# Performance work log

Measured on AMD Instinct MI355X. Metric: run time of the kernel, lower is better.

The kernel has to match this reference:

```python
import jax, jax.numpy as jnp
import numpy as np

B, S, D, H = 4, 1024, 1024, 16
HD = D // H  # 64, even for RoPE


def _rope_tables(seq_len, head_dim):
    inv_freq = 1.0 / (10000.0 ** (jnp.arange(0, head_dim, 2, dtype=jnp.float32) / head_dim))
    pos = jnp.arange(seq_len, dtype=jnp.float32)
    ang = pos[:, None] * inv_freq[None, :]           # [S, HD/2]
    return jnp.cos(ang), jnp.sin(ang)


def _apply_rope(x, cos, sin):
    # x: [B, S, H, HD]; cos/sin: [S, HD/2] broadcast to [1, S, 1, HD/2]
    c = cos[None, :, None, :]
    s = sin[None, :, None, :]
    x1 = x[..., 0::2]
    x2 = x[..., 1::2]
    return jnp.concatenate([x1 * c - x2 * s, x1 * s + x2 * c], axis=-1)


def setup_inputs() -> dict:
    key = jax.random.key(0)
    ks = jax.random.split(key, 11)
    sc = 1.0 / np.sqrt(D)
    inp = {
        "query": jax.random.normal(ks[0], (B, S, D), jnp.float32),
        "key": jax.random.normal(ks[1], (B, S, D), jnp.float32),
        "value": jax.random.normal(ks[2], (B, S, D), jnp.float32),
        "mask": jnp.tril(jnp.ones((S, S), jnp.int32))[None, None],  # causal [1,1,S,S]
        "Wq": jax.random.normal(ks[3], (D, D), jnp.float32) * sc,
        "bq": jnp.zeros((D,), jnp.float32),
        "Wk": jax.random.normal(ks[4], (D, D), jnp.float32) * sc,
        "bk": jnp.zeros((D,), jnp.float32),
        "Wv": jax.random.normal(ks[5], (D, D), jnp.float32) * sc,
        "bv": jnp.zeros((D,), jnp.float32),
        "Wo": jax.random.normal(ks[6], (D, D), jnp.float32) * sc,
        "bo": jnp.zeros((D,), jnp.float32),
    }
    return inp


def reference(query, key, value, mask, Wq, bq, Wk, bk, Wv, bv, Wo, bo):
    Bq, Sq, _ = query.shape
    Sk = key.shape[1]
    q = (query @ Wq + bq).reshape(Bq, Sq, H, HD)
    k = (key @ Wk + bk).reshape(Bq, Sk, H, HD)
    v = (value @ Wv + bv).reshape(Bq, Sk, H, HD)
    cos, sin = _rope_tables(max(Sq, Sk), HD)
    q = _apply_rope(q, cos[:Sq], sin[:Sq])
    k = _apply_rope(k, cos[:Sk], sin[:Sk])
    scores = jnp.einsum("bqhd,bkhd->bhqk", q, k) / jnp.sqrt(jnp.float32(HD))
    scores = jnp.where(mask == 0, jnp.float32(-jnp.inf), scores)
    attn = jax.nn.softmax(scores, axis=-1)  # dropout p=0 (inference)
    ctx = jnp.einsum("bhqk,bkhd->bqhd", attn, v).reshape(Bq, Sq, D)
    return ctx @ Wo + bo
```

## Files before the change

### kernel.cpp

```cpp
#include <hip/hip_runtime.h>
#include <hip/hip_bf16.h>
#include <math.h>

#define B_DIM 4
#define S_DIM 1024
#define D_DIM 1024
#define H_DIM 16
#define HD_DIM 64
#define M_TOT 4096

typedef short short8 __attribute__((ext_vector_type(8)));
typedef float f32x4 __attribute__((ext_vector_type(4)));

__device__ inline float bf2f(short u)
{
    return __uint_as_float(((unsigned)(unsigned short)u) << 16);
}

__device__ inline void gload_lds16(const void* gsrc, void* lds)
{
    __builtin_amdgcn_global_load_lds(
        (const __attribute__((address_space(1))) unsigned int*)gsrc,
        (__attribute__((address_space(3))) unsigned int*)lds, 16, 0, 0);
}

__global__ __launch_bounds__(256) void rope_table_kernel(float* __restrict__ tab)
{
    const int t = blockIdx.x * 256 + threadIdx.x;
    const int pos = t >> 5, i = t & 31;
    float inv = powf(10000.0f, -(float)(2 * i) / 64.0f);
    float ang = (float)pos * inv;
    float s, c;
    sincosf(ang, &s, &c);
    tab[t] = c;
    tab[32768 + t] = s;
}

__global__ __launch_bounds__(256) void transpose4_to_bf16_kernel(
    const float* __restrict__ W0, const float* __restrict__ W1,
    const float* __restrict__ W2, const float* __restrict__ W3,
    __hip_bfloat16* __restrict__ T0, __hip_bfloat16* __restrict__ T1,
    __hip_bfloat16* __restrict__ T2, __hip_bfloat16* __restrict__ T3)
{
    const float* W = (blockIdx.z == 0) ? W0 : (blockIdx.z == 1) ? W1
                    : (blockIdx.z == 2) ? W2 : W3;
    __hip_bfloat16* T = (blockIdx.z == 0) ? T0 : (blockIdx.z == 1) ? T1
                       : (blockIdx.z == 2) ? T2 : T3;

    __shared__ float tile[32][33];
    const int tid = threadIdx.x;
    const int r = tid >> 3;
    const int c4 = (tid & 7) * 4;

    float4 v = *(const float4*)&W[(long)(blockIdx.y * 32 + r) * D_DIM + blockIdx.x * 32 + c4];
    tile[r][c4 + 0] = v.x;
    tile[r][c4 + 1] = v.y;
    tile[r][c4 + 2] = v.z;
    tile[r][c4 + 3] = v.w;
    __syncthreads();

    __hip_bfloat16 o[4];
    o[0] = __float2bfloat16(tile[c4 + 0][r]);
    o[1] = __float2bfloat16(tile[c4 + 1][r]);
    o[2] = __float2bfloat16(tile[c4 + 2][r]);
    o[3] = __float2bfloat16(tile[c4 + 3][r]);
    *(uint2*)&T[(long)(blockIdx.x * 32 + r) * D_DIM + blockIdx.y * 32 + c4] = *(uint2*)o;
}

__global__ __launch_bounds__(256, 3) void gemm_qkv_kernel(
    const float* __restrict__ Xq, const float* __restrict__ Xk,
    const float* __restrict__ Xv,
    const __hip_bfloat16* __restrict__ WtQ, const __hip_bfloat16* __restrict__ WtK,
    const __hip_bfloat16* __restrict__ WtV,
    const float* __restrict__ bq, const float* __restrict__ bk,
    const float* __restrict__ bv,
    __hip_bfloat16* __restrict__ Qo, __hip_bfloat16* __restrict__ Ko,
    __hip_bfloat16* __restrict__ Vto,
    const float* __restrict__ tab)
{
    __shared__ __align__(16) __hip_bfloat16 Al[2][128][40];
    __shared__ __align__(16) __hip_bfloat16 Bl[2][128][32];

    const int F = blockIdx.x + 8 * blockIdx.y + 256 * blockIdx.z;
    const int xcd = F & 7;
    const int sb = F >> 3;
    const int z = sb >> 5;
    const int n0 = (sb & 7) * 128;
    const int m0 = ((xcd << 2) | ((sb >> 3) & 3)) * 128;

    const float* X = (z == 0) ? Xq : (z == 1) ? Xk : Xv;
    const __hip_bfloat16* Wt = (z == 0) ? WtQ : (z == 1) ? WtK : WtV;
    const float* bias = (z == 0) ? bq : (z == 1) ? bk : bv;

    const int tid = threadIdx.x;
    const int l = tid & 63;
    const int w = tid >> 6;

    const int srow = w * 16 + (l >> 2);
    const int sk = ((l & 3) ^ ((l >> 2) & 3)) * 8;
    const __hip_bfloat16* Bbase = Wt + (long)(n0 + srow) * D_DIM + sk;

    const int arow = tid >> 1;
    const int ak = (tid & 1) * 16;
    const float* Af = X + (long)(m0 + arow) * D_DIM + ak;

    const int lrow = l & 15;
    const int kg = l >> 4;
    const int ksw = (kg ^ (lrow & 3)) * 8;
    const int wr = (w >> 1) * 64;
    const int wc = (w & 1) * 64;

    f32x4 acc[4][4];
#pragma unroll
    for (int i = 0; i < 4; ++i)
#pragma unroll
        for (int j = 0; j < 4; ++j) acc[i][j] = (f32x4){0.f, 0.f, 0.f, 0.f};

    {
        char* ldsB = (char*)&Bl[0][0][0] + w * 1024;
        gload_lds16(Bbase, ldsB);
        gload_lds16(Bbase + 64 * D_DIM, ldsB + 4096);
        float4 f0 = *(const float4*)(Af);
        float4 f1 = *(const float4*)(Af + 4);
        float4 f2 = *(const float4*)(Af + 8);
        float4 f3 = *(const float4*)(Af + 12);
        float fa[16] = {f0.x, f0.y, f0.z, f0.w, f1.x, f1.y, f1.z, f1.w,
                        f2.x, f2.y, f2.z, f2.w, f3.x, f3.y, f3.z, f3.w};
        __attribute__((aligned(16))) __hip_bfloat16 ab[16];
#pragma unroll
        for (int i = 0; i < 16; ++i) ab[i] = __float2bfloat16(fa[i]);
        *(short8*)&Al[0][arow][ak]     = ((const short8*)ab)[0];
        *(short8*)&Al[0][arow][ak + 8] = ((const short8*)ab)[1];
    }
    __syncthreads();

#pragma unroll 2
    for (int t = 0; t < 32; ++t) {
        const int cur = t & 1;
        const int nxt = cur ^ 1;
        const bool more = (t < 31);

        float4 f0, f1, f2, f3;
        if (more) {
            const int k0n = (t + 1) * 32;
            char* ldsB = (char*)&Bl[nxt][0][0] + w * 1024;
            gload_lds16(Bbase + k0n, ldsB);
            gload_lds16(Bbase + 64 * D_DIM + k0n, ldsB + 4096);
            f0 = *(const float4*)(Af + k0n);
            f1 = *(const float4*)(Af + k0n + 4);
            f2 = *(const float4*)(Af + k0n + 8);
            f3 = *(const float4*)(Af + k0n + 12);
        }

        short8 af[4], bf[4];
#pragma unroll
        for (int i = 0; i < 4; ++i)
            af[i] = *(const short8*)&Al[cur][wr + i * 16 + lrow][kg * 8];
#pragma unroll
        for (int j = 0; j < 4; ++j)
            bf[j] = *(const short8*)&Bl[cur][wc + j * 16 + lrow][ksw];
#pragma unroll
        for (int i = 0; i < 4; ++i)
#pragma unroll
            for (int j = 0; j < 4; ++j)
                acc[i][j] = __builtin_amdgcn_mfma_f32_16x16x32_bf16(
                    af[i], bf[j], acc[i][j], 0, 0, 0);

        if (more) {
            float fa[16] = {f0.x, f0.y, f0.z, f0.w, f1.x, f1.y, f1.z, f1.w,
                            f2.x, f2.y, f2.z, f2.w, f3.x, f3.y, f3.z, f3.w};
            __attribute__((aligned(16))) __hip_bfloat16 ab[16];
#pragma unroll
            for (int i = 0; i < 16; ++i) ab[i] = __float2bfloat16(fa[i]);
            *(short8*)&Al[nxt][arow][ak]     = ((const short8*)ab)[0];
            *(short8*)&Al[nxt][arow][ak + 8] = ((const short8*)ab)[1];
        }
        __syncthreads();
    }

    if (z < 2) {
        __hip_bfloat16* Out = (z == 0) ? Qo : Ko;
        const float scale = (z == 0) ? 0.125f : 1.0f;
#pragma unroll
        for (int i = 0; i < 4; ++i) {
#pragma unroll
            for (int j = 0; j < 4; ++j) {
                const int col = n0 + wc + j * 16 + lrow;
                const float bvs = bias[col];
                const int odd = col & 1;
                const int ip = (col & 63) >> 1;
                const int ocol = (col & ~63) + ip + (odd ? 32 : 0);
                const int rbase = m0 + wr + i * 16 + kg * 4;
#pragma unroll
                for (int r = 0; r < 4; ++r) {
                    const int row = rbase + r;
                    const int pos = row & (S_DIM - 1);
                    float x = acc[i][j][r] + bvs;
                    float xo = __shfl_xor(x, 1);
                    float x1 = odd ? xo : x;
                    float x2 = odd ? x : xo;
                    float cv = tab[pos * 32 + ip];
                    float sv = tab[32768 + pos * 32 + ip];
                    float res = odd ? (x1 * sv + x2 * cv) : (x1 * cv - x2 * sv);
                    Out[(long)row * D_DIM + ocol] = __float2bfloat16(res * scale);
                }
            }
        }
    } else {
#pragma unroll
        for (int i = 0; i < 4; ++i) {
#pragma unroll
            for (int j = 0; j < 4; ++j) {
                const int col = n0 + wc + j * 16 + lrow;
                const float bvs = bias[col];
                const int hh = col >> 6, dd = col & 63;
                const int rbase = m0 + wr + i * 16 + kg * 4;
                const int bb = rbase >> 10, s0 = rbase & 1023;
                __hip_bfloat16 o[4];
#pragma unroll
                for (int r = 0; r < 4; ++r)
                    o[r] = __float2bfloat16(acc[i][j][r] + bvs);
                *(uint2*)&Vto[((long)((bb * H_DIM + hh) * HD_DIM + dd)) * S_DIM + s0] =
                    *(uint2*)o;
            }
        }
    }
}

__global__ __launch_bounds__(256, 2) void gemm_wo_kernel(
    const __hip_bfloat16* __restrict__ X, const __hip_bfloat16* __restrict__ Wt,
    const float* __restrict__ bias, float* __restrict__ Out)
{
    __shared__ __align__(16) __hip_bfloat16 Al[2][128][32];
    __shared__ __align__(16) __hip_bfloat16 Bl[2][64][32];

    const int F = blockIdx.x;
    const int xcd = F & 7;
    const int s = F >> 3;
    const int n0 = (s & 15) * 64;
    const int m0 = ((xcd << 2) | (s >> 4)) * 128;

    const int tid = threadIdx.x;
    const int l = tid & 63;
    const int w = tid >> 6;

    const int srow = w * 16 + (l >> 2);
    const int sk = ((l & 3) ^ ((l >> 2) & 3)) * 8;
    const __hip_bfloat16* Abase = X + (long)(m0 + srow) * D_DIM + sk;
    const __hip_bfloat16* Bbase = Wt + (long)(n0 + srow) * D_DIM + sk;

    const int lrow = l & 15;
    const int kg = l >> 4;
    const int ksw = (kg ^ (lrow & 3)) * 8;
    const int wr = (w >> 1) * 64;
    const int wc = (w & 1) * 32;

    f32x4 acc[4][2];
#pragma unroll
    for (int i = 0; i < 4; ++i)
#pragma unroll
        for (int j = 0; j < 2; ++j) acc[i][j] = (f32x4){0.f, 0.f, 0.f, 0.f};

    {
        char* ldsA = (char*)&Al[0][0][0] + w * 1024;
        char* ldsB = (char*)&Bl[0][0][0] + w * 1024;
        gload_lds16(Abase, ldsA);
        gload_lds16(Abase + 64 * D_DIM, ldsA + 4096);
        gload_lds16(Bbase, ldsB);
    }
    __syncthreads();

#pragma unroll 2
    for (int t = 0; t < 32; ++t) {
        const int cur = t & 1;
        const int nxt = cur ^ 1;
        if (t < 31) {
            const int k0n = (t + 1) * 32;
            char* ldsA = (char*)&Al[nxt][0][0] + w * 1024;
            char* ldsB = (char*)&Bl[nxt][0][0] + w * 1024;
            gload_lds16(Abase + k0n, ldsA);
            gload_lds16(Abase + 64 * D_DIM + k0n, ldsA + 4096);
            gload_lds16(Bbase + k0n, ldsB);
        }

        short8 af[4], bf[2];
#pragma unroll
        for (int i = 0; i < 4; ++i)
            af[i] = *(const short8*)&Al[cur][wr + i * 16 + lrow][ksw];
#pragma unroll
        for (int j = 0; j < 2; ++j)
            bf[j] = *(const short8*)&Bl[cur][wc + j * 16 + lrow][ksw];
#pragma unroll
        for (int i = 0; i < 4; ++i)
#pragma unroll
            for (int j = 0; j < 2; ++j)
                acc[i][j] = __builtin_amdgcn_mfma_f32_16x16x32_bf16(
                    af[i], bf[j], acc[i][j], 0, 0, 0);
        __syncthreads();
    }

#pragma unroll
    for (int i = 0; i < 4; ++i) {
#pragma unroll
        for (int j = 0; j < 2; ++j) {
            const int col = n0 + wc + j * 16 + lrow;
            const float bv = bias[col];
            const int rbase = m0 + wr + i * 16 + kg * 4;
#pragma unroll
            for (int r = 0; r < 4; ++r)
                Out[(long)(rbase + r) * D_DIM + col] = acc[i][j][r] + bv;
        }
    }
}

#define KPAD 72

__global__ __launch_bounds__(256, 2) void attn_mfma_kernel(
    const __hip_bfloat16* __restrict__ Q,
    const __hip_bfloat16* __restrict__ K,
    const __hip_bfloat16* __restrict__ Vt,
    __hip_bfloat16* __restrict__ CTX)
{
    __shared__ __align__(16) __hip_bfloat16 Kl[64][KPAD];
    __shared__ __align__(16) __hip_bfloat16 Vl[64][KPAD];
    __shared__ __align__(16) __hip_bfloat16 Pl[4][32][KPAD];
    __shared__ __align__(16) float aS[4][2][16];

    const int tid = threadIdx.x;
    const int l = tid & 63;
    const int w = tid >> 6;

    const int bid = blockIdx.x + 8 * blockIdx.y + 128 * blockIdx.z;
    const int half = bid >> 8;
    const int idx = bid & 255;
    int qt = idx & 7;
    if (half) qt = 7 - qt;
    const int rest = idx >> 3;
    const int h = rest & 15;
    const int b = (rest >> 4) | (half << 1);

    const int lrow = l & 15;
    const int kg = l >> 4;
    const int kg4 = kg * 4;

    const int q0w = qt * 128 + w * 32;
    const long qrow_base = (long)b * S_DIM + q0w;

    short8 qf[2][2];
#pragma unroll
    for (int m = 0; m < 2; ++m)
#pragma unroll
        for (int ks = 0; ks < 2; ++ks)
            qf[m][ks] = *(const short8*)&Q[(qrow_base + m * 16 + lrow) * D_DIM +
                                           h * HD_DIM + ks * 32 + kg * 8];

    f32x4 ctx[2][4];
#pragma unroll
    for (int m = 0; m < 2; ++m)
#pragma unroll
        for (int d = 0; d < 4; ++d) ctx[m][d] = (f32x4){0.f, 0.f, 0.f, 0.f};
    float mrun[2] = {-1e30f, -1e30f};
    float lrun[2] = {0.f, 0.f};

    const int sr = tid >> 2;
    const int sc2 = (tid & 3) * 16;
    const __hip_bfloat16* Kg = K + ((long)b * S_DIM + sr) * D_DIM + h * HD_DIM + sc2;
    const __hip_bfloat16* Vg = Vt + ((long)((b * H_DIM + h) * HD_DIM) + sr) * S_DIM + sc2;

    const int ktmax = 2 * qt + 1;

    short8 kp0 = *(const short8*)Kg;
    short8 kp1 = *(const short8*)(Kg + 8);
    short8 vp0 = *(const short8*)Vg;
    short8 vp1 = *(const short8*)(Vg + 8);

    for (int kt = 0; kt <= ktmax; ++kt) {
        __syncthreads();
        *(short8*)&Kl[sr][sc2]     = kp0;
        *(short8*)&Kl[sr][sc2 + 8] = kp1;
        *(short8*)&Vl[sr][sc2]     = vp0;
        *(short8*)&Vl[sr][sc2 + 8] = vp1;
        if (kt < ktmax) {
            const __hip_bfloat16* kp = Kg + (long)(kt + 1) * 64 * D_DIM;
            const __hip_bfloat16* vp = Vg + (kt + 1) * 64;
            kp0 = *(const short8*)kp;
            kp1 = *(const short8*)(kp + 8);
            vp0 = *(const short8*)vp;
            vp1 = *(const short8*)(vp + 8);
        }
        __syncthreads();

        if (kt * 64 > q0w + 31) continue;

        f32x4 sac[2][4];
#pragma unroll
        for (int m = 0; m < 2; ++m)
#pragma unroll
            for (int nt = 0; nt < 4; ++nt) sac[m][nt] = (f32x4){0.f, 0.f, 0.f, 0.f};

        short8 kf[4][2];
#pragma unroll
        for (int nt = 0; nt < 4; ++nt)
#pragma unroll
            for (int ks = 0; ks < 2; ++ks)
                kf[nt][ks] = *(const short8*)&Kl[nt * 16 + lrow][ks * 32 + kg * 8];
#pragma unroll
        for (int m = 0; m < 2; ++m)
#pragma unroll
            for (int nt = 0; nt < 4; ++nt)
#pragma unroll
                for (int ks = 0; ks < 2; ++ks)
                    sac[m][nt] = __builtin_amdgcn_mfma_f32_16x16x32_bf16(
                        kf[nt][ks], qf[m][ks], sac[m][nt], 0, 0, 0);

        const bool partial = (kt * 64 + 63 > q0w);
        const int kbase = kt * 64;
#pragma unroll
        for (int m = 0; m < 2; ++m) {
            const int qg = q0w + m * 16 + lrow;
            float s[16];
#pragma unroll
            for (int nt = 0; nt < 4; ++nt)
#pragma unroll
                for (int r = 0; r < 4; ++r) {
                    float v = sac[m][nt][r];
                    if (partial && (kbase + nt * 16 + kg4 + r > qg)) v = -1e30f;
                    s[nt * 4 + r] = v;
                }
            float t8[8];
#pragma unroll
            for (int i = 0; i < 8; ++i) t8[i] = fmaxf(s[i], s[i + 8]);
#pragma unroll
            for (int i = 0; i < 4; ++i) t8[i] = fmaxf(t8[i], t8[i + 4]);
            float mx = fmaxf(fmaxf(t8[0], t8[1]), fmaxf(t8[2], t8[3]));
            mx = fmaxf(mx, __shfl_xor(mx, 16));
            mx = fmaxf(mx, __shfl_xor(mx, 32));
            const float mnew = fmaxf(mrun[m], mx);
            const float alpha = __expf(mrun[m] - mnew);
            mrun[m] = mnew;

            float p0s = 0.f, p1s = 0.f, p2s = 0.f, p3s = 0.f;
            __attribute__((aligned(8))) __hip_bfloat16 pb[16];
#pragma unroll
            for (int i = 0; i < 4; ++i) {
                float p = __expf(s[i] - mnew);      p0s += p; pb[i] = __float2bfloat16(p);
            }
#pragma unroll
            for (int i = 4; i < 8; ++i) {
                float p = __expf(s[i] - mnew);      p1s += p; pb[i] = __float2bfloat16(p);
            }
#pragma unroll
            for (int i = 8; i < 12; ++i) {
                float p = __expf(s[i] - mnew);      p2s += p; pb[i] = __float2bfloat16(p);
            }
#pragma unroll
            for (int i = 12; i < 16; ++i) {
                float p = __expf(s[i] - mnew);      p3s += p; pb[i] = __float2bfloat16(p);
            }
            float sum = (p0s + p1s) + (p2s + p3s);
            sum += __shfl_xor(sum, 16);
            sum += __shfl_xor(sum, 32);
            lrun[m] = lrun[m] * alpha + sum;

            if (kg == 0) aS[w][m][lrow] = alpha;
#pragma unroll
            for (int nt = 0; nt < 4; ++nt)
                *(uint2*)&Pl[w][m * 16 + lrow][nt * 16 + kg4] = *(uint2*)&pb[nt * 4];
        }

#pragma unroll
        for (int m = 0; m < 2; ++m) {
            f32x4 al4 = *(const f32x4*)&aS[w][m][kg4];
#pragma unroll
            for (int dt = 0; dt < 4; ++dt)
#pragma unroll
                for (int r = 0; r < 4; ++r) ctx[m][dt][r] *= al4[r];
        }

        short8 vf[4][2];
#pragma unroll
        for (int dt = 0; dt < 4; ++dt)
#pragma unroll
            for (int ks = 0; ks < 2; ++ks)
                vf[dt][ks] = *(const short8*)&Vl[dt * 16 + lrow][ks * 32 + kg * 8];
#pragma unroll
        for (int m = 0; m < 2; ++m) {
            short8 pf[2];
#pragma unroll
            for (int ks = 0; ks < 2; ++ks)
                pf[ks] = *(const short8*)&Pl[w][m * 16 + lrow][ks * 32 + kg * 8];
#pragma unroll
            for (int dt = 0; dt < 4; ++dt)
#pragma unroll
                for (int ks = 0; ks < 2; ++ks)
                    ctx[m][dt] = __builtin_amdgcn_mfma_f32_16x16x32_bf16(
                        pf[ks], vf[dt][ks], ctx[m][dt], 0, 0, 0);
        }
    }

    if (kg == 0) {
        aS[w][0][lrow] = lrun[0];
        aS[w][1][lrow] = lrun[1];
    }
#pragma unroll
    for (int m = 0; m < 2; ++m) {
        f32x4 lv = *(const f32x4*)&aS[w][m][kg4];
#pragma unroll
        for (int r = 0; r < 4; ++r) {
            const float inv_l = 1.0f / lv[r];
            const long rowoff = (qrow_base + m * 16 + kg4 + r) * D_DIM + h * HD_DIM;
#pragma unroll
            for (int dt = 0; dt < 4; ++dt)
                CTX[rowoff + dt * 16 + lrow] = __float2bfloat16(ctx[m][dt][r] * inv_l);
        }
    }
}

extern "C" void kernel_launch(void* const* d_in, const int* in_sizes, int n_in,
                              void* d_out, int out_size, void* d_ws, size_t ws_size,
                              hipStream_t stream)
{
    const float* query = (const float*)d_in[0];
    const float* key   = (const float*)d_in[1];
    const float* value = (const float*)d_in[2];
    const float* Wq = (const float*)d_in[4];
    const float* bq = (const float*)d_in[5];
    const float* Wk = (const float*)d_in[6];
    const float* bk = (const float*)d_in[7];
    const float* Wv = (const float*)d_in[8];
    const float* bv = (const float*)d_in[9];
    const float* Wo = (const float*)d_in[10];
    const float* bo = (const float*)d_in[11];

    char* wsb = (char*)d_ws;
    __hip_bfloat16* Qr    = (__hip_bfloat16*)(wsb);
    __hip_bfloat16* Kr    = (__hip_bfloat16*)(wsb + (8L  << 20));
    __hip_bfloat16* Vtb   = (__hip_bfloat16*)(wsb + (16L << 20));
    __hip_bfloat16* CTXbf = (__hip_bfloat16*)(wsb + (24L << 20));
    __hip_bfloat16* WtQ   = (__hip_bfloat16*)(wsb + (32L << 20));
    __hip_bfloat16* WtK   = (__hip_bfloat16*)(wsb + (34L << 20));
    __hip_bfloat16* WtV   = (__hip_bfloat16*)(wsb + (36L << 20));
    __hip_bfloat16* WtO   = (__hip_bfloat16*)(wsb + (38L << 20));
    float*          tab   = (float*)(wsb + (40L << 20));

    rope_table_kernel<<<128, 256, 0, stream>>>(tab);
    transpose4_to_bf16_kernel<<<dim3(32, 32, 4), 256, 0, stream>>>(
        Wq, Wk, Wv, Wo, WtQ, WtK, WtV, WtO);

    gemm_qkv_kernel<<<dim3(8, 32, 3), 256, 0, stream>>>(
        query, key, value, WtQ, WtK, WtV, bq, bk, bv, Qr, Kr, Vtb, tab);

    attn_mfma_kernel<<<dim3(8, 16, 4), 256, 0, stream>>>(Qr, Kr, Vtb, CTXbf);

    gemm_wo_kernel<<<512, 256, 0, stream>>>(CTXbf, WtO, bo, (float*)d_out);
}
```

Measured before the change: 132.9 us.

## Replace double-buffered LDS pipeline with single buffer and change XOR swizzle

Both projection GEMM kernels drop their two-stage LDS double buffering for a single buffer. Each k-step now fills the buffer and brackets the fill with two barriers, so global-to-LDS loads no longer overlap MFMA work on the previous tile. The B-tile swizzle changes from (row&3) to ((row>>1)&3) to alter the bank-conflict pattern. Halving LDS may raise occupancy, but it adds a barrier per iteration and exposes load latency.

```diff
diff --git a/kernel.cpp b/kernel.cpp
--- a/kernel.cpp
+++ b/kernel.cpp
@@ -78,8 +78,8 @@
     __hip_bfloat16* __restrict__ Vto,
     const float* __restrict__ tab)
 {
-    __shared__ __align__(16) __hip_bfloat16 Al[2][128][40];
-    __shared__ __align__(16) __hip_bfloat16 Bl[2][128][32];
+    __shared__ __align__(16) __hip_bfloat16 Al[128][40];
+    __shared__ __align__(16) __hip_bfloat16 Bl[128][32];
 
     const int F = blockIdx.x + 8 * blockIdx.y + 256 * blockIdx.z;
     const int xcd = F & 7;
@@ -97,8 +97,9 @@
     const int w = tid >> 6;
 
     const int srow = w * 16 + (l >> 2);
-    const int sk = ((l & 3) ^ ((l >> 2) & 3)) * 8;
+    const int sk = ((l & 3) ^ ((l >> 3) & 3)) * 8;
     const __hip_bfloat16* Bbase = Wt + (long)(n0 + srow) * D_DIM + sk;
+    char* ldsB0 = (char*)&Bl[0][0] + w * 1024;
 
     const int arow = tid >> 1;
     const int ak = (tid & 1) * 16;
@@ -106,7 +107,7 @@
 
     const int lrow = l & 15;
     const int kg = l >> 4;
-    const int ksw = (kg ^ (lrow & 3)) * 8;
+    const int ksw = (kg ^ ((lrow >> 1) & 3)) * 8;
     const int wr = (w >> 1) * 64;
     const int wc = (w & 1) * 64;
 
@@ -116,66 +117,45 @@
 #pragma unroll
         for (int j = 0; j < 4; ++j) acc[i][j] = (f32x4){0.f, 0.f, 0.f, 0.f};
 
-    {
-        char* ldsB = (char*)&Bl[0][0][0] + w * 1024;
-        gload_lds16(Bbase, ldsB);
-        gload_lds16(Bbase + 64 * D_DIM, ldsB + 4096);
-        float4 f0 = *(const float4*)(Af);
-        float4 f1 = *(const float4*)(Af + 4);
-        float4 f2 = *(const float4*)(Af + 8);
-        float4 f3 = *(const float4*)(Af + 12);
+    float4 f0 = *(const float4*)(Af);
+    float4 f1 = *(const float4*)(Af + 4);
+    float4 f2 = *(const float4*)(Af + 8);
+    float4 f3 = *(const float4*)(Af + 12);
+
+    for (int k0 = 0; k0 < D_DIM; k0 += 32) {
         float fa[16] = {f0.x, f0.y, f0.z, f0.w, f1.x, f1.y, f1.z, f1.w,
                         f2.x, f2.y, f2.z, f2.w, f3.x, f3.y, f3.z, f3.w};
         __attribute__((aligned(16))) __hip_bfloat16 ab[16];
 #pragma unroll
         for (int i = 0; i < 16; ++i) ab[i] = __float2bfloat16(fa[i]);
-        *(short8*)&Al[0][arow][ak]     = ((const short8*)ab)[0];
-        *(short8*)&Al[0][arow][ak + 8] = ((const short8*)ab)[1];
-    }
-    __syncthreads();
-
-#pragma unroll 2
-    for (int t = 0; t < 32; ++t) {
-        const int cur = t & 1;
-        const int nxt = cur ^ 1;
-        const bool more = (t < 31);
-
-        float4 f0, f1, f2, f3;
-        if (more) {
-            const int k0n = (t + 1) * 32;
-            char* ldsB = (char*)&Bl[nxt][0][0] + w * 1024;
-            gload_lds16(Bbase + k0n, ldsB);
-            gload_lds16(Bbase + 64 * D_DIM + k0n, ldsB + 4096);
-            f0 = *(const float4*)(Af + k0n);
-            f1 = *(const float4*)(Af + k0n + 4);
-            f2 = *(const float4*)(Af + k0n + 8);
-            f3 = *(const float4*)(Af + k0n + 12);
+
+        __syncthreads();
+        *(short8*)&Al[arow][ak]     = ((const short8*)ab)[0];
+        *(short8*)&Al[arow][ak + 8] = ((const short8*)ab)[1];
+        gload_lds16(Bbase + k0, ldsB0);
+        gload_lds16(Bbase + 64 * D_DIM + k0, ldsB0 + 4096);
+        __syncthreads();
+
+        if (k0 + 32 < D_DIM) {
+            f0 = *(const float4*)(Af + k0 + 32);
+            f1 = *(const float4*)(Af + k0 + 36);
+            f2 = *(const float4*)(Af + k0 + 40);
+            f3 = *(const float4*)(Af + k0 + 44);
         }
 
         short8 af[4], bf[4];
 #pragma unroll
         for (int i = 0; i < 4; ++i)
-            af[i] = *(const short8*)&Al[cur][wr + i * 16 + lrow][kg * 8];
+            af[i] = *(const short8*)&Al[wr + i * 16 + lrow][kg * 8];
 #pragma unroll
         for (int j = 0; j < 4; ++j)
-            bf[j] = *(const short8*)&Bl[cur][wc + j * 16 + lrow][ksw];
+            bf[j] = *(const short8*)&Bl[wc + j * 16 + lrow][ksw];
 #pragma unroll
         for (int i = 0; i < 4; ++i)
 #pragma unroll
             for (int j = 0; j < 4; ++j)
                 acc[i][j] = __builtin_amdgcn_mfma_f32_16x16x32_bf16(
                     af[i], bf[j], acc[i][j], 0, 0, 0);
-
-        if (more) {
-            float fa[16] = {f0.x, f0.y, f0.z, f0.w, f1.x, f1.y, f1.z, f1.w,
-                            f2.x, f2.y, f2.z, f2.w, f3.x, f3.y, f3.z, f3.w};
-            __attribute__((aligned(16))) __hip_bfloat16 ab[16];
-#pragma unroll
-            for (int i = 0; i < 16; ++i) ab[i] = __float2bfloat16(fa[i]);
-            *(short8*)&Al[nxt][arow][ak]     = ((const short8*)ab)[0];
-            *(short8*)&Al[nxt][arow][ak + 8] = ((const short8*)ab)[1];
-        }
-        __syncthreads();
     }
 
     if (z < 2) {
@@ -231,8 +211,8 @@
     const __hip_bfloat16* __restrict__ X, const __hip_bfloat16* __restrict__ Wt,
     const float* __restrict__ bias, float* __restrict__ Out)
 {
-    __shared__ __align__(16) __hip_bfloat16 Al[2][128][32];
-    __shared__ __align__(16) __hip_bfloat16 Bl[2][64][32];
+    __shared__ __align__(16) __hip_bfloat16 Al[128][32];
+    __shared__ __align__(16) __hip_bfloat16 Bl[64][32];
 
     const int F = blockIdx.x;
     const int xcd = F & 7;
@@ -245,13 +225,15 @@
     const int w = tid >> 6;
 
     const int srow = w * 16 + (l >> 2);
-    const int sk = ((l & 3) ^ ((l >> 2) & 3)) * 8;
+    const int sk = ((l & 3) ^ ((l >> 3) & 3)) * 8;
     const __hip_bfloat16* Abase = X + (long)(m0 + srow) * D_DIM + sk;
     const __hip_bfloat16* Bbase = Wt + (long)(n0 + srow) * D_DIM + sk;
+    char* ldsA0 = (char*)&Al[0][0] + w * 1024;
+    char* ldsB0 = (char*)&Bl[0][0] + w * 1024;
 
     const int lrow = l & 15;
     const int kg = l >> 4;
-    const int ksw = (kg ^ (lrow & 3)) * 8;
+    const int ksw = (kg ^ ((lrow >> 1) & 3)) * 8;
     const int wr = (w >> 1) * 64;
     const int wc = (w & 1) * 32;
 
@@ -261,42 +243,26 @@
 #pragma unroll
         for (int j = 0; j < 2; ++j) acc[i][j] = (f32x4){0.f, 0.f, 0.f, 0.f};
 
-    {
-        char* ldsA = (char*)&Al[0][0][0] + w * 1024;
-        char* ldsB = (char*)&Bl[0][0][0] + w * 1024;
-        gload_lds16(Abase, ldsA);
-        gload_lds16(Abase + 64 * D_DIM, ldsA + 4096);
-        gload_lds16(Bbase, ldsB);
-    }
-    __syncthreads();
-
-#pragma unroll 2
-    for (int t = 0; t < 32; ++t) {
-        const int cur = t & 1;
-        const int nxt = cur ^ 1;
-        if (t < 31) {
-            const int k0n = (t + 1) * 32;
-            char* ldsA = (char*)&Al[nxt][0][0] + w * 1024;
-            char* ldsB = (char*)&Bl[nxt][0][0] + w * 1024;
-            gload_lds16(Abase + k0n, ldsA);
-            gload_lds16(Abase + 64 * D_DIM + k0n, ldsA + 4096);
-            gload_lds16(Bbase + k0n, ldsB);
-        }
+    for (int k0 = 0; k0 < D_DIM; k0 += 32) {
+        __syncthreads();
+        gload_lds16(Abase + k0, ldsA0);
+        gload_lds16(Abase + 64 * D_DIM + k0, ldsA0 + 4096);
+        gload_lds16(Bbase + k0, ldsB0);
+        __syncthreads();
 
         short8 af[4], bf[2];
 #pragma unroll
         for (int i = 0; i < 4; ++i)
-            af[i] = *(const short8*)&Al[cur][wr + i * 16 + lrow][ksw];
+            af[i] = *(const short8*)&Al[wr + i * 16 + lrow][ksw];
 #pragma unroll
         for (int j = 0; j < 2; ++j)
-            bf[j] = *(const short8*)&Bl[cur][wc + j * 16 + lrow][ksw];
+            bf[j] = *(const short8*)&Bl[wc + j * 16 + lrow][ksw];
 #pragma unroll
         for (int i = 0; i < 4; ++i)
 #pragma unroll
             for (int j = 0; j < 2; ++j)
                 acc[i][j] = __builtin_amdgcn_mfma_f32_16x16x32_bf16(
                     af[i], bf[j], acc[i][j], 0, 0, 0);
-        __syncthreads();
     }
 
 #pragma unroll
```

New measurement: 120.5 us. -9.3%, faster.
